# Performance work log

Hardware: AMD Instinct MI355X
Metric: run time of the kernel (lower is better)

The kernel has to match this reference:

```python
import jax, jax.numpy as jnp
import numpy as np

B, A, H, L = 4096, 4096, 768, 4  # batch, num_atoms, hidden_dim, antecedent_len


def setup_inputs() -> dict:
    key = jax.random.key(0)
    ks = jax.random.split(key, 10)
    s = 0.02
    cls = jax.random.normal(ks[0], (B, H), jnp.float32)
    x_ = jax.random.bernoulli(ks[1], 0.5, (B, A)).astype(jnp.float32)
    gru_w_ih = jax.random.normal(ks[2], (3 * H, H), jnp.float32) * s
    gru_w_hh = jax.random.normal(ks[3], (3 * H, H), jnp.float32) * s
    gru_b_ih = jax.random.normal(ks[4], (3 * H,), jnp.float32) * s
    gru_b_hh = jax.random.normal(ks[5], (3 * H,), jnp.float32) * s
    head_w = jax.random.normal(ks[6], (A, H), jnp.float32) * s
    head_b = jax.random.normal(ks[7], (A,), jnp.float32) * s
    ae_weight = jax.random.normal(ks[8], (A, H), jnp.float32) * s
    return {"cls": cls, "x_": x_, "gru_w_ih": gru_w_ih, "gru_w_hh": gru_w_hh,
            "gru_b_ih": gru_b_ih, "gru_b_hh": gru_b_hh, "head_w": head_w,
            "head_b": head_b, "ae_weight": ae_weight}


def _gru_step(x, h, w_ih, w_hh, b_ih, b_hh):
    # torch GRU gate order: r, z, n
    gi = x @ w_ih.T + b_ih          # [B, 3H]
    gh = h @ w_hh.T + b_hh
    i_r, i_z, i_n = jnp.split(gi, 3, axis=-1)
    h_r, h_z, h_n = jnp.split(gh, 3, axis=-1)
    r = jax.nn.sigmoid(i_r + h_r)
    z = jax.nn.sigmoid(i_z + h_z)
    n = jnp.tanh(i_n + r * h_n)
    return (1.0 - z) * n + z * h


def reference(cls, x_, gru_w_ih, gru_w_hh, gru_b_ih, gru_b_hh, head_w, head_b, ae_weight):
    key = jax.random.key(42)
    mask = x_
    h = jnp.zeros_like(cls)
    cur_input = cls
    max_index = None
    rows = jnp.arange(B)
    probs = []
    for j in range(L):
        h = _gru_step(cur_input, h, gru_w_ih, gru_w_hh, gru_b_ih, gru_b_hh)
        out = h @ head_w.T + head_b  # [B, A]  (dropout = identity in eval)
        # filtered_softmax mask update (mutations persist across steps)
        if j == 0:
            empty = jnp.sum(mask, axis=-1) == 0.0
            mask = mask.at[:, 0].set(jnp.where(empty, 1.0, mask[:, 0]))
        else:
            mask = jnp.where((max_index == 0)[:, None], 0.0, mask)
            mask = mask.at[:, 0].set(1.0)
        logits = jnp.where(mask > 0, out, -jnp.inf)
        # hard gumbel-softmax, tau=1 (straight-through)
        key, sub = jax.random.split(key)
        g = jax.random.gumbel(sub, logits.shape, logits.dtype)
        y_soft = jax.nn.softmax(logits + g, axis=1)
        idx = jnp.argmax(y_soft, axis=1)
        y_hard = jax.nn.one_hot(idx, A, dtype=y_soft.dtype)
        prob = y_hard + y_soft - jax.lax.stop_gradient(y_soft)
        max_index = idx
        # scatter zeros at the selected atom (remove from candidate set)
        mask = mask.at[rows, idx].set(0.0)
        probs.append(prob)
        atom_wsum = prob @ jax.lax.stop_gradient(ae_weight)  # [B, H]
        cur_input = cls + atom_wsum
    return jnp.stack(probs, axis=1)  # [B, L, A]
```

## Files before the change

### kernel.cpp

```cpp
#include <hip/hip_runtime.h>
#include <cstdint>
#include <cstddef>
#include <math.h>


#define KB 4096
#define KA 4096
#define KH 768
#define KL 4

typedef __attribute__((ext_vector_type(8))) short bf16x8;
typedef __attribute__((ext_vector_type(4))) float f32x4;

__host__ __device__ inline unsigned rotl32(unsigned x, int d) {
  return (x << d) | (x >> (32 - d));
}

__host__ __device__ inline void tf2x32(unsigned k0, unsigned k1,
                                       unsigned x0, unsigned x1,
                                       unsigned& o0, unsigned& o1) {
  unsigned ks2 = k0 ^ k1 ^ 0x1BD11BDAu;
  x0 += k0; x1 += k1;
#define TF_R(r) { x0 += x1; x1 = rotl32(x1, (r)); x1 ^= x0; }
  TF_R(13) TF_R(15) TF_R(26) TF_R(6)
  x0 += k1;  x1 += ks2 + 1u;
  TF_R(17) TF_R(29) TF_R(16) TF_R(24)
  x0 += ks2; x1 += k0 + 2u;
  TF_R(13) TF_R(15) TF_R(26) TF_R(6)
  x0 += k0;  x1 += k1 + 3u;
  TF_R(17) TF_R(29) TF_R(16) TF_R(24)
  x0 += k1;  x1 += ks2 + 4u;
  TF_R(13) TF_R(15) TF_R(26) TF_R(6)
  x0 += ks2; x1 += k0 + 5u;
#undef TF_R
  o0 = x0; o1 = x1;
}

__device__ inline ushort f2bf(float f) {
  unsigned u = __float_as_uint(f);
  unsigned r = (u + 0x7fffu + ((u >> 16) & 1u)) >> 16;
  return (ushort)r;
}
__device__ inline float bf2f(ushort h) {
  return __uint_as_float(((unsigned)h) << 16);
}

__device__ inline float gumbel_at(unsigned s0, unsigned s1, unsigned ctr) {
  unsigned o0, o1;
  tf2x32(s0, s1, 0u, ctr, o0, o1);
  unsigned bits = o0 ^ o1;
  float f = __uint_as_float((bits >> 9) | 0x3f800000u) - 1.0f;
  const float TINY = 1.17549435e-38f;
  float u = fmaxf(TINY, f + TINY);
  return -logf(-logf(u));
}

#define GLDS(gp, lp) \
  __builtin_amdgcn_global_load_lds( \
      (const __attribute__((address_space(1))) void*)(gp), \
      (__attribute__((address_space(3))) void*)(lp), 16, 0, 0)

__global__ __launch_bounds__(256) void gemm3_nt(
    const ushort* __restrict__ Ahi, const ushort* __restrict__ Alo,
    const ushort* __restrict__ Bhi, const ushort* __restrict__ Blo,
    float* __restrict__ C, long long ldc) {
  __shared__ ushort smem[4 * 128 * 32];
  const int tid = threadIdx.x;
  const int wave = tid >> 6;
  const int lane = tid & 63;
  const long long bm = (long long)blockIdx.y * 128;
  const long long bn = (long long)blockIdx.x * 128;
  const int wm = (wave & 1) * 64;
  const int wn = (wave >> 1) * 64;

  f32x4 acc[4][4];
#pragma unroll
  for (int i = 0; i < 4; ++i)
#pragma unroll
    for (int j = 0; j < 4; ++j) acc[i][j] = (f32x4){0.f, 0.f, 0.f, 0.f};

  const int r = lane >> 2;
  const int cs = lane & 3;
  const int csrc = cs ^ ((r & 3) ^ ((r >> 2) & 3));
  const int m15 = lane & 15;
  const int kg = (lane >> 4) & 3;
  const int slot = kg ^ ((m15 & 3) ^ ((m15 >> 2) & 3));

  for (int kt = 0; kt < 24; ++kt) {
    const int k0 = kt * 32;
#pragma unroll
    for (int s = 0; s < 2; ++s) {
      const int m0 = wave * 32 + s * 16;
      const long long arow = (bm + m0 + r) * KH + k0 + csrc * 8;
      const long long brow = (bn + m0 + r) * KH + k0 + csrc * 8;
      GLDS(Ahi + arow, &smem[0 * 4096 + m0 * 32]);
      GLDS(Alo + arow, &smem[1 * 4096 + m0 * 32]);
      GLDS(Bhi + brow, &smem[2 * 4096 + m0 * 32]);
      GLDS(Blo + brow, &smem[3 * 4096 + m0 * 32]);
    }
    __syncthreads();
    bf16x8 bh[4], bl[4];
#pragma unroll
    for (int jj = 0; jj < 4; ++jj) {
      const int n = wn + jj * 16 + m15;
      bh[jj] = *(const bf16x8*)&smem[2 * 4096 + n * 32 + slot * 8];
      bl[jj] = *(const bf16x8*)&smem[3 * 4096 + n * 32 + slot * 8];
    }
#pragma unroll
    for (int i = 0; i < 4; ++i) {
      const int m = wm + i * 16 + m15;
      bf16x8 ah = *(const bf16x8*)&smem[0 * 4096 + m * 32 + slot * 8];
      bf16x8 al = *(const bf16x8*)&smem[1 * 4096 + m * 32 + slot * 8];
#pragma unroll
      for (int jj = 0; jj < 4; ++jj) {
        acc[i][jj] = __builtin_amdgcn_mfma_f32_16x16x32_bf16(ah, bh[jj], acc[i][jj], 0, 0, 0);
        acc[i][jj] = __builtin_amdgcn_mfma_f32_16x16x32_bf16(ah, bl[jj], acc[i][jj], 0, 0, 0);
        acc[i][jj] = __builtin_amdgcn_mfma_f32_16x16x32_bf16(al, bh[jj], acc[i][jj], 0, 0, 0);
      }
    }
    __syncthreads();
  }
  const int rq = (lane >> 4) * 4;
#pragma unroll
  for (int i = 0; i < 4; ++i)
#pragma unroll
    for (int j = 0; j < 4; ++j) {
      const long long n = bn + wn + j * 16 + m15;
#pragma unroll
      for (int rg = 0; rg < 4; ++rg) {
        const long long m = bm + wm + i * 16 + rq + rg;
        C[m * ldc + n] = acc[i][j][rg];
      }
    }
}

__global__ __launch_bounds__(256) void gemm_fused(
    const ushort* __restrict__ hHi, const ushort* __restrict__ hLo,
    const ushort* __restrict__ WhhHi, const ushort* __restrict__ WhhLo,
    float* __restrict__ Gh, const ushort* __restrict__ HwHi,
    const float* __restrict__ head_b, ushort* __restrict__ Vbuf, int gh_nb) {
  __shared__ ushort smem[4 * 128 * 32];
  const int tid = threadIdx.x;
  const int wave = tid >> 6;
  const int lane = tid & 63;
  const int bid = blockIdx.x;
  const int wm = (wave & 1) * 64;
  const int wn = (wave >> 1) * 64;
  const int r = lane >> 2;
  const int cs = lane & 3;
  const int csrc = cs ^ ((r & 3) ^ ((r >> 2) & 3));
  const int m15 = lane & 15;
  const int kg = (lane >> 4) & 3;
  const int slot = kg ^ ((m15 & 3) ^ ((m15 >> 2) & 3));

  f32x4 acc[4][4];
#pragma unroll
  for (int i = 0; i < 4; ++i)
#pragma unroll
    for (int j = 0; j < 4; ++j) acc[i][j] = (f32x4){0.f, 0.f, 0.f, 0.f};

  if (bid < gh_nb) {
    const long long bm = (long long)(bid / 18) * 128;
    const long long bn = (long long)(bid % 18) * 128;
    for (int kt = 0; kt < 24; ++kt) {
      const int k0 = kt * 32;
#pragma unroll
      for (int s = 0; s < 2; ++s) {
        const int m0 = wave * 32 + s * 16;
        const long long arow = (bm + m0 + r) * KH + k0 + csrc * 8;
        const long long brow = (bn + m0 + r) * KH + k0 + csrc * 8;
        GLDS(hHi + arow, &smem[0 * 4096 + m0 * 32]);
        GLDS(hLo + arow, &smem[1 * 4096 + m0 * 32]);
        GLDS(WhhHi + brow, &smem[2 * 4096 + m0 * 32]);
        GLDS(WhhLo + brow, &smem[3 * 4096 + m0 * 32]);
      }
      __syncthreads();
      bf16x8 bh[4], bl[4];
#pragma unroll
      for (int jj = 0; jj < 4; ++jj) {
        const int n = wn + jj * 16 + m15;
        bh[jj] = *(const bf16x8*)&smem[2 * 4096 + n * 32 + slot * 8];
        bl[jj] = *(const bf16x8*)&smem[3 * 4096 + n * 32 + slot * 8];
      }
#pragma unroll
      for (int i = 0; i < 4; ++i) {
        const int m = wm + i * 16 + m15;
        bf16x8 ah = *(const bf16x8*)&smem[0 * 4096 + m * 32 + slot * 8];
        bf16x8 al = *(const bf16x8*)&smem[1 * 4096 + m * 32 + slot * 8];
#pragma unroll
        for (int jj = 0; jj < 4; ++jj) {
          acc[i][jj] = __builtin_amdgcn_mfma_f32_16x16x32_bf16(ah, bh[jj], acc[i][jj], 0, 0, 0);
          acc[i][jj] = __builtin_amdgcn_mfma_f32_16x16x32_bf16(ah, bl[jj], acc[i][jj], 0, 0, 0);
          acc[i][jj] = __builtin_amdgcn_mfma_f32_16x16x32_bf16(al, bh[jj], acc[i][jj], 0, 0, 0);
        }
      }
      __syncthreads();
    }
    const int rq = (lane >> 4) * 4;
#pragma unroll
    for (int i = 0; i < 4; ++i)
#pragma unroll
      for (int j = 0; j < 4; ++j) {
        const long long n = bn + wn + j * 16 + m15;
#pragma unroll
        for (int rg = 0; rg < 4; ++rg) {
          const long long m = bm + wm + i * 16 + rq + rg;
          Gh[m * (3 * KH) + n] = acc[i][j][rg];
        }
      }
  } else {
    const int k = bid - gh_nb;
    const long long bm = (long long)(k >> 5) * 128;
    const long long bn = (long long)(k & 31) * 128;
    for (int kt = 0; kt < 24; ++kt) {
      const int k0 = kt * 32;
#pragma unroll
      for (int s = 0; s < 2; ++s) {
        const int m0 = wave * 32 + s * 16;
        const long long arow = (bm + m0 + r) * KH + k0 + csrc * 8;
        const long long brow = (bn + m0 + r) * KH + k0 + csrc * 8;
        GLDS(hHi + arow, &smem[0 * 4096 + m0 * 32]);
        GLDS(HwHi + brow, &smem[1 * 4096 + m0 * 32]);
      }
      __syncthreads();
      bf16x8 bh[4];
#pragma unroll
      for (int jj = 0; jj < 4; ++jj) {
        const int n = wn + jj * 16 + m15;
        bh[jj] = *(const bf16x8*)&smem[1 * 4096 + n * 32 + slot * 8];
      }
#pragma unroll
      for (int i = 0; i < 4; ++i) {
        const int m = wm + i * 16 + m15;
        bf16x8 ah = *(const bf16x8*)&smem[0 * 4096 + m * 32 + slot * 8];
#pragma unroll
        for (int jj = 0; jj < 4; ++jj)
          acc[i][jj] = __builtin_amdgcn_mfma_f32_16x16x32_bf16(ah, bh[jj], acc[i][jj], 0, 0, 0);
      }
      __syncthreads();
    }
    const int rq = (lane >> 4) * 4;
#pragma unroll
    for (int i = 0; i < 4; ++i)
#pragma unroll
      for (int j = 0; j < 4; ++j) {
        const long long n = bn + wn + j * 16 + m15;
        const float hb = head_b[n];
#pragma unroll
        for (int rg = 0; rg < 4; ++rg) {
          const long long m = bm + wm + i * 16 + rq + rg;
          Vbuf[m * KA + n] = f2bf(acc[i][j][rg] + hb);
        }
      }
  }
}

#define CUM1 442368
#define CUM2 884736
#define CUM3 1671168
#define CUM4 2457600
#define CUM5 3244032
#define PREP_CONV_BLOCKS 12672

__global__ void prep(const float* __restrict__ w_ih, const float* __restrict__ w_hh,
                     const float* __restrict__ head_w, const float* __restrict__ cls,
                     const float* __restrict__ ae_w, const float* __restrict__ x_,
                     ushort* __restrict__ WihHi, ushort* __restrict__ WihLo,
                     ushort* __restrict__ WhhHi, ushort* __restrict__ WhhLo,
                     ushort* __restrict__ HwHi, ushort* __restrict__ CAhi,
                     ushort* __restrict__ CAlo, unsigned char* __restrict__ empty) {
  const int blk = blockIdx.x;
  const int tid = threadIdx.x;
  if (blk < PREP_CONV_BLOCKS) {
    const int i = blk * 256 + tid;
    const float* src; ushort* dhi; ushort* dlo; int base; int split; int ofs = 0;
    if (i < CUM1)      { src = w_ih;   dhi = WihHi; dlo = WihLo; base = 0;    split = 1; }
    else if (i < CUM2) { src = w_hh;   dhi = WhhHi; dlo = WhhLo; base = CUM1; split = 1; }
    else if (i < CUM3) { src = head_w; dhi = HwHi;  dlo = 0;     base = CUM2; split = 0; }
    else if (i < CUM4) { src = cls;    dhi = CAhi;  dlo = CAlo;  base = CUM3; split = 1; }
    else               { src = ae_w;   dhi = CAhi;  dlo = CAlo;  base = CUM4; split = 1; ofs = 786432; }
    const int k = i - base;
    float4 v = ((const float4*)src)[k];
    ushort4 h;
    h.x = f2bf(v.x); h.y = f2bf(v.y); h.z = f2bf(v.z); h.w = f2bf(v.w);
    ((ushort4*)dhi)[ofs + k] = h;
    if (split) {
      ushort4 l;
      l.x = f2bf(v.x - bf2f(h.x)); l.y = f2bf(v.y - bf2f(h.y));
      l.z = f2bf(v.z - bf2f(h.z)); l.w = f2bf(v.w - bf2f(h.w));
      ((ushort4*)dlo)[ofs + k] = l;
    }
  } else {
    const int row = blk - PREP_CONV_BLOCKS;
    __shared__ int scnt[256];
    const float4* xr = (const float4*)(x_ + (size_t)row * KA);
    int cnt = 0;
#pragma unroll
    for (int k = 0; k < 4; ++k) {
      float4 v = xr[tid + (k << 8)];
      cnt += (v.x != 0.f) + (v.y != 0.f) + (v.z != 0.f) + (v.w != 0.f);
    }
    scnt[tid] = cnt;
    __syncthreads();
    for (int s = 128; s > 0; s >>= 1) {
      if (tid < s) scnt[tid] += scnt[tid + s];
      __syncthreads();
    }
    if (tid == 0) empty[row] = (scnt[0] == 0) ? 1 : 0;
  }
}

__global__ void gru_gate2(const float* __restrict__ PAE, const float* __restrict__ Gh,
                          const int* __restrict__ idxbuf,
                          const float* __restrict__ b_ih, const float* __restrict__ b_hh,
                          float* __restrict__ h, ushort* __restrict__ hHi,
                          ushort* __restrict__ hLo, int first) {
  int i4 = blockIdx.x * 256 + threadIdx.x;
  int b = i4 / (KH / 4);
  int c4 = i4 - b * (KH / 4);
  const f32x4* gp = (const f32x4*)(PAE + (size_t)b * (3 * KH));
  f32x4 ir = gp[c4], iz = gp[c4 + 192], inn = gp[c4 + 384];
  const f32x4* bi = (const f32x4*)b_ih;
  const f32x4* bhh = (const f32x4*)b_hh;
  f32x4 hr = bhh[c4], hz = bhh[c4 + 192], hn = bhh[c4 + 384];
  f32x4 hp = (f32x4){0.f, 0.f, 0.f, 0.f};
  if (!first) {
    const f32x4* ga = (const f32x4*)(PAE + ((size_t)KB + idxbuf[b]) * (3 * KH));
    ir += ga[c4]; iz += ga[c4 + 192]; inn += ga[c4 + 384];
    const f32x4* gh = (const f32x4*)(Gh + (size_t)b * (3 * KH));
    hr += gh[c4]; hz += gh[c4 + 192]; hn += gh[c4 + 384];
    hp = ((const f32x4*)h)[i4];
  }
  ir += bi[c4]; iz += bi[c4 + 192]; inn += bi[c4 + 384];
  f32x4 hv;
  ushort4 hh, hl;
  ushort* hhp = &hh.x;
  ushort* hlp = &hl.x;
#pragma unroll
  for (int e = 0; e < 4; ++e) {
    float rr = 1.f / (1.f + expf(-(ir[e] + hr[e])));
    float z = 1.f / (1.f + expf(-(iz[e] + hz[e])));
    float n = tanhf(inn[e] + rr * hn[e]);
    float v = (1.f - z) * n + z * hp[e];
    hv[e] = v;
    ushort hb = f2bf(v);
    hhp[e] = hb;
    hlp[e] = f2bf(v - bf2f(hb));
  }
  ((f32x4*)h)[i4] = hv;
  ((ushort4*)hHi)[i4] = hh;
  ((ushort4*)hLo)[i4] = hl;
}

__global__ __launch_bounds__(256) void sample_step(
    float* __restrict__ out, const ushort* __restrict__ Vbuf,
    const float* __restrict__ x_, unsigned char* __restrict__ mask,
    int* __restrict__ idxbuf, const float* __restrict__ hbuf,
    const float* __restrict__ head_w, const float* __restrict__ head_b,
    const unsigned char* __restrict__ empty, int j, unsigned s0, unsigned s1) {
  const int b = blockIdx.x;
  const int tid = threadIdx.x;
  float* orow = out + ((size_t)b * KL + j) * KA;
  unsigned char* mrow = mask + (size_t)b * KA;
  const ushort* vrow = Vbuf + (size_t)b * KA;
  const float4* xrow4 = (const float4*)(x_ + (size_t)b * KA);
  __shared__ float sv[256];
  __shared__ int scand[16];
  __shared__ float srefined[16];
  __shared__ int scnt;
  __shared__ int ssel;
  const float EPS = 0.02f;

  if (tid == 0) scnt = 0;

  const int idx_prev = (j > 0) ? idxbuf[b] : 0;
  const int emp = (j == 0) ? empty[b] : 0;

  float vreg[16];
  unsigned mbits = 0;
  float lmax = -INFINITY;
#pragma unroll
  for (int k = 0; k < 2; ++k) {
    const int ci = tid + (k << 8);
    const int abase = ci * 8;
    uint4 vv = ((const uint4*)vrow)[ci];
    unsigned vw[4] = {vv.x, vv.y, vv.z, vv.w};
    float xv[8];
    unsigned mw0 = 0, mw1 = 0;
    if (j == 0) {
      float4 x0 = xrow4[ci * 2], x1 = xrow4[ci * 2 + 1];
      xv[0] = x0.x; xv[1] = x0.y; xv[2] = x0.z; xv[3] = x0.w;
      xv[4] = x1.x; xv[5] = x1.y; xv[6] = x1.z; xv[7] = x1.w;
    } else {
      uint2 mwv = ((const uint2*)mrow)[ci];
      mw0 = mwv.x; mw1 = mwv.y;
    }
#pragma unroll
    for (int e = 0; e < 8; ++e) {
      const int a = abase + e;
      int m;
      if (j == 0) {
        m = (xv[e] != 0.f) || (emp && a == 0);
      } else {
        unsigned mb = (e < 4) ? ((mw0 >> (8 * e)) & 0xffu)
                              : ((mw1 >> (8 * (e - 4))) & 0xffu);
        m = (a == 0) || (idx_prev != 0 && mb);
      }
      float v = -INFINITY;
      if (m) {
        ushort hv16 = (ushort)((vw[e >> 1] >> (16 * (e & 1))) & 0xffffu);
        float g = gumbel_at(s0, s1, (unsigned)(b * KA + a));
        v = bf2f(hv16) + g;
        mbits |= (1u << (k * 8 + e));
      }
      vreg[k * 8 + e] = v;
      lmax = fmaxf(lmax, v);
    }
  }
  sv[tid] = lmax;
  __syncthreads();
  for (int s = 128; s > 0; s >>= 1) {
    if (tid < s) sv[tid] = fmaxf(sv[tid], sv[tid + s]);
    __syncthreads();
  }
  const float vmax = sv[0];

  const float thresh = vmax - EPS;
#pragma unroll
  for (int k = 0; k < 2; ++k)
#pragma unroll
    for (int e = 0; e < 8; ++e) {
      if (vreg[k * 8 + e] >= thresh) {
        int slot = atomicAdd(&scnt, 1);
        if (slot < 16) scand[slot] = (tid + (k << 8)) * 8 + e;
      }
    }
  __syncthreads();
  const int ncand = min(scnt, 16);

  {
    const int wv = tid >> 6;
    const int lane = tid & 63;
    const float4* h4 = (const float4*)(hbuf + (size_t)b * KH);
    for (int t = wv; t < ncand; t += 4) {
      const int a = scand[t];
      const float4* w4 = (const float4*)(head_w + (size_t)a * KH);
      float sum = 0.f;
#pragma unroll
      for (int u = 0; u < 3; ++u) {
        float4 hv = h4[lane + u * 64];
        float4 wv4 = w4[lane + u * 64];
        sum = fmaf(hv.x, wv4.x, sum);
        sum = fmaf(hv.y, wv4.y, sum);
        sum = fmaf(hv.z, wv4.z, sum);
        sum = fmaf(hv.w, wv4.w, sum);
      }
#pragma unroll
      for (int off = 32; off > 0; off >>= 1) sum += __shfl_down(sum, off);
      if (lane == 0) {
        float g = gumbel_at(s0, s1, (unsigned)(b * KA + a));
        srefined[t] = sum + head_b[a] + g;
      }
    }
  }
  __syncthreads();

  if (tid == 0) {
    float best = -INFINITY;
    int bsel = KA;
    for (int t = 0; t < ncand; ++t) {
      float v = srefined[t];
      int a = scand[t];
      if (v > best || (v == best && a < bsel)) { best = v; bsel = a; }
    }
    ssel = bsel;
  }
  __syncthreads();
  const int sel = ssel;

#pragma unroll
  for (int k = 0; k < 2; ++k) {
    const int ci = tid + (k << 8);
    const int abase = ci * 8;
    unsigned mw[2] = {0u, 0u};
    float ov[8];
#pragma unroll
    for (int e = 0; e < 8; ++e) {
      const int a = abase + e;
      int m = (mbits >> (k * 8 + e)) & 1;
      if (a == sel) m = 0;
      mw[e >> 2] |= ((unsigned)m) << (8 * (e & 3));
      ov[e] = (a == sel) ? 1.f : 0.f;
    }
    ((uint2*)mrow)[ci] = make_uint2(mw[0], mw[1]);
    ((float4*)orow)[ci * 2]     = make_float4(ov[0], ov[1], ov[2], ov[3]);
    ((float4*)orow)[ci * 2 + 1] = make_float4(ov[4], ov[5], ov[6], ov[7]);
  }
  if (tid == 0) idxbuf[b] = sel;
}

extern "C" void kernel_launch(void* const* d_in, const int* in_sizes, int n_in,
                              void* d_out, int out_size, void* d_ws, size_t ws_size,
                              hipStream_t stream) {
  const float* cls    = (const float*)d_in[0];
  const float* x_     = (const float*)d_in[1];
  const float* w_ih   = (const float*)d_in[2];
  const float* w_hh   = (const float*)d_in[3];
  const float* b_ih   = (const float*)d_in[4];
  const float* b_hh   = (const float*)d_in[5];
  const float* head_w = (const float*)d_in[6];
  const float* head_b = (const float*)d_in[7];
  const float* ae_w   = (const float*)d_in[8];
  float* out = (float*)d_out;

  char* p = (char*)d_ws;
  ushort* CAhi  = (ushort*)p; p += (size_t)2 * KB * KH * 2;
  ushort* CAlo  = (ushort*)p; p += (size_t)2 * KB * KH * 2;
  ushort* WihHi = (ushort*)p; p += (size_t)3 * KH * KH * 2;
  ushort* WihLo = (ushort*)p; p += (size_t)3 * KH * KH * 2;
  ushort* WhhHi = (ushort*)p; p += (size_t)3 * KH * KH * 2;
  ushort* WhhLo = (ushort*)p; p += (size_t)3 * KH * KH * 2;
  ushort* HwHi  = (ushort*)p; p += (size_t)KA * KH * 2;
  ushort* hHi   = (ushort*)p; p += (size_t)KB * KH * 2;
  ushort* hLo   = (ushort*)p; p += (size_t)KB * KH * 2;
  float*  hbuf  = (float*)p;  p += (size_t)KB * KH * 4;
  float*  PAE   = (float*)p;  p += (size_t)2 * KB * 3 * KH * 4;
  float*  Gh    = (float*)p;  p += (size_t)KB * 3 * KH * 4;
  ushort* Vbuf  = (ushort*)p; p += (size_t)KB * KA * 2;
  unsigned char* mask  = (unsigned char*)p; p += (size_t)KB * KA;
  unsigned char* empty = (unsigned char*)p; p += (size_t)KB;
  int* idxbuf = (int*)p; p += (size_t)KB * 4;

  unsigned key0 = 0u, key1 = 42u;
  unsigned sub0[KL], sub1[KL];
  for (int j = 0; j < KL; ++j) {
    unsigned n0, n1, t0, t1;
    tf2x32(key0, key1, 0u, 0u, n0, n1);
    tf2x32(key0, key1, 0u, 1u, t0, t1);
    sub0[j] = t0; sub1[j] = t1;
    key0 = n0; key1 = n1;
  }

  prep<<<PREP_CONV_BLOCKS + KB, 256, 0, stream>>>(
      w_ih, w_hh, head_w, cls, ae_w, x_,
      WihHi, WihLo, WhhHi, WhhLo, HwHi, CAhi, CAlo, empty);
  gemm3_nt<<<dim3(3 * KH / 128, 2 * KB / 128), 256, 0, stream>>>(
      CAhi, CAlo, WihHi, WihLo, PAE, 3 * KH);

  for (int j = 0; j < KL; ++j) {
    gru_gate2<<<KB * KH / 4 / 256, 256, 0, stream>>>(PAE, Gh, idxbuf, b_ih, b_hh,
                                                     hbuf, hHi, hLo, j == 0);
    const int gh_nb = (j < KL - 1) ? 576 : 0;
    gemm_fused<<<gh_nb + 1024, 256, 0, stream>>>(
        hHi, hLo, WhhHi, WhhLo, Gh, HwHi, head_b, Vbuf, gh_nb);
    sample_step<<<KB, 256, 0, stream>>>(out, Vbuf, x_, mask, idxbuf, hbuf,
                                        head_w, head_b, empty, j, sub0[j], sub1[j]);
  }
}
```

Baseline: 1.029 ms.

## Fuse GRU gate update into sampling kernel and add occupancy hints to GEMMs

Moves the per-step GRU gate computation for steps after the first into the tail of the sampling kernel, using the freshly chosen index directly instead of reloading it from global memory. This removes one kernel launch per step and a full pass over the gate buffers. A separate first-step gate kernel handles the zero-hidden case. It also adds a min-blocks-per-CU hint of 4 to both GEMM kernels, which may force the compiler to limit register use and could cause spills.

After: 954.9 us, median of 3. 7.2% less time.

```diff
diff --git a/kernel.cpp b/kernel.cpp
--- a/kernel.cpp
+++ b/kernel.cpp
@@ -60,7 +60,7 @@
       (const __attribute__((address_space(1))) void*)(gp), \
       (__attribute__((address_space(3))) void*)(lp), 16, 0, 0)
 
-__global__ __launch_bounds__(256) void gemm3_nt(
+__global__ __launch_bounds__(256, 4) void gemm3_nt(
     const ushort* __restrict__ Ahi, const ushort* __restrict__ Alo,
     const ushort* __restrict__ Bhi, const ushort* __restrict__ Blo,
     float* __restrict__ C, long long ldc) {
@@ -134,7 +134,7 @@
     }
 }
 
-__global__ __launch_bounds__(256) void gemm_fused(
+__global__ __launch_bounds__(256, 4) void gemm_fused(
     const ushort* __restrict__ hHi, const ushort* __restrict__ hLo,
     const ushort* __restrict__ WhhHi, const ushort* __restrict__ WhhLo,
     float* __restrict__ Gh, const ushort* __restrict__ HwHi,
@@ -310,28 +310,20 @@
   }
 }
 
-__global__ void gru_gate2(const float* __restrict__ PAE, const float* __restrict__ Gh,
-                          const int* __restrict__ idxbuf,
+__global__ void gru_gate0(const float* __restrict__ PAE,
                           const float* __restrict__ b_ih, const float* __restrict__ b_hh,
                           float* __restrict__ h, ushort* __restrict__ hHi,
-                          ushort* __restrict__ hLo, int first) {
+                          ushort* __restrict__ hLo) {
   int i4 = blockIdx.x * 256 + threadIdx.x;
   int b = i4 / (KH / 4);
   int c4 = i4 - b * (KH / 4);
   const f32x4* gp = (const f32x4*)(PAE + (size_t)b * (3 * KH));
-  f32x4 ir = gp[c4], iz = gp[c4 + 192], inn = gp[c4 + 384];
   const f32x4* bi = (const f32x4*)b_ih;
   const f32x4* bhh = (const f32x4*)b_hh;
+  f32x4 ir = gp[c4] + bi[c4];
+  f32x4 iz = gp[c4 + 192] + bi[c4 + 192];
+  f32x4 inn = gp[c4 + 384] + bi[c4 + 384];
   f32x4 hr = bhh[c4], hz = bhh[c4 + 192], hn = bhh[c4 + 384];
-  f32x4 hp = (f32x4){0.f, 0.f, 0.f, 0.f};
-  if (!first) {
-    const f32x4* ga = (const f32x4*)(PAE + ((size_t)KB + idxbuf[b]) * (3 * KH));
-    ir += ga[c4]; iz += ga[c4 + 192]; inn += ga[c4 + 384];
-    const f32x4* gh = (const f32x4*)(Gh + (size_t)b * (3 * KH));
-    hr += gh[c4]; hz += gh[c4 + 192]; hn += gh[c4 + 384];
-    hp = ((const f32x4*)h)[i4];
-  }
-  ir += bi[c4]; iz += bi[c4 + 192]; inn += bi[c4 + 384];
   f32x4 hv;
   ushort4 hh, hl;
   ushort* hhp = &hh.x;
@@ -341,7 +333,7 @@
     float rr = 1.f / (1.f + expf(-(ir[e] + hr[e])));
     float z = 1.f / (1.f + expf(-(iz[e] + hz[e])));
     float n = tanhf(inn[e] + rr * hn[e]);
-    float v = (1.f - z) * n + z * hp[e];
+    float v = (1.f - z) * n;
     hv[e] = v;
     ushort hb = f2bf(v);
     hhp[e] = hb;
@@ -352,12 +344,16 @@
   ((ushort4*)hLo)[i4] = hl;
 }
 
-__global__ __launch_bounds__(256) void sample_step(
+__global__ __launch_bounds__(256) void sample_gate(
     float* __restrict__ out, const ushort* __restrict__ Vbuf,
     const float* __restrict__ x_, unsigned char* __restrict__ mask,
-    int* __restrict__ idxbuf, const float* __restrict__ hbuf,
+    int* __restrict__ idxbuf, float* __restrict__ hbuf,
     const float* __restrict__ head_w, const float* __restrict__ head_b,
-    const unsigned char* __restrict__ empty, int j, unsigned s0, unsigned s1) {
+    const unsigned char* __restrict__ empty,
+    const float* __restrict__ PAE, const float* __restrict__ Gh,
+    const float* __restrict__ b_ih, const float* __restrict__ b_hh,
+    ushort* __restrict__ hHi, ushort* __restrict__ hLo,
+    int j, int do_gate, unsigned s0, unsigned s1) {
   const int b = blockIdx.x;
   const int tid = threadIdx.x;
   float* orow = out + ((size_t)b * KL + j) * KA;
@@ -497,6 +493,41 @@
     ((float4*)orow)[ci * 2 + 1] = make_float4(ov[4], ov[5], ov[6], ov[7]);
   }
   if (tid == 0) idxbuf[b] = sel;
+
+  if (do_gate && tid < 192) {
+    const int c4 = tid;
+    const int i4 = b * (KH / 4) + c4;
+    const f32x4* gp = (const f32x4*)(PAE + (size_t)b * (3 * KH));
+    const f32x4* ga = (const f32x4*)(PAE + ((size_t)KB + sel) * (3 * KH));
+    const f32x4* bi = (const f32x4*)b_ih;
+    const f32x4* bhh = (const f32x4*)b_hh;
+    const f32x4* gh4 = (const f32x4*)(Gh + (size_t)b * (3 * KH));
+    f32x4 ir = gp[c4] + ga[c4] + bi[c4];
+    f32x4 iz = gp[c4 + 192] + ga[c4 + 192] + bi[c4 + 192];
+    f32x4 inn = gp[c4 + 384] + ga[c4 + 384] + bi[c4 + 384];
+    f32x4 hr = bhh[c4] + gh4[c4];
+    f32x4 hz = bhh[c4 + 192] + gh4[c4 + 192];
+    f32x4 hn = bhh[c4 + 384] + gh4[c4 + 384];
+    f32x4 hp = ((const f32x4*)hbuf)[i4];
+    f32x4 hv;
+    ushort4 hh, hl;
+    ushort* hhp = &hh.x;
+    ushort* hlp = &hl.x;
+#pragma unroll
+    for (int e = 0; e < 4; ++e) {
+      float rr = 1.f / (1.f + expf(-(ir[e] + hr[e])));
+      float z = 1.f / (1.f + expf(-(iz[e] + hz[e])));
+      float n = tanhf(inn[e] + rr * hn[e]);
+      float v = (1.f - z) * n + z * hp[e];
+      hv[e] = v;
+      ushort hb = f2bf(v);
+      hhp[e] = hb;
+      hlp[e] = f2bf(v - bf2f(hb));
+    }
+    ((f32x4*)hbuf)[i4] = hv;
+    ((ushort4*)hHi)[i4] = hh;
+    ((ushort4*)hLo)[i4] = hl;
+  }
 }
 
 extern "C" void kernel_launch(void* const* d_in, const int* in_sizes, int n_in,
@@ -546,14 +577,16 @@
       WihHi, WihLo, WhhHi, WhhLo, HwHi, CAhi, CAlo, empty);
   gemm3_nt<<<dim3(3 * KH / 128, 2 * KB / 128), 256, 0, stream>>>(
       CAhi, CAlo, WihHi, WihLo, PAE, 3 * KH);
+  gru_gate0<<<KB * KH / 4 / 256, 256, 0, stream>>>(PAE, b_ih, b_hh,
+                                                   hbuf, hHi, hLo);
 
   for (int j = 0; j < KL; ++j) {
-    gru_gate2<<<KB * KH / 4 / 256, 256, 0, stream>>>(PAE, Gh, idxbuf, b_ih, b_hh,
-                                                     hbuf, hHi, hLo, j == 0);
     const int gh_nb = (j < KL - 1) ? 576 : 0;
     gemm_fused<<<gh_nb + 1024, 256, 0, stream>>>(
         hHi, hLo, WhhHi, WhhLo, Gh, HwHi, head_b, Vbuf, gh_nb);
-    sample_step<<<KB, 256, 0, stream>>>(out, Vbuf, x_, mask, idxbuf, hbuf,
-                                        head_w, head_b, empty, j, sub0[j], sub1[j]);
-  }
-}
+    sample_gate<<<KB, 256, 0, stream>>>(
+        out, Vbuf, x_, mask, idxbuf, hbuf, head_w, head_b, empty,
+        PAE, Gh, b_ih, b_hh, hHi, hLo, j, (j < KL - 1) ? 1 : 0,
+        sub0[j], sub1[j]);
+  }
+}
```
